# Performance work log

Measured on AMD Instinct MI355X. Metric: run time of the kernel, lower is better.

The kernel has to match this reference:

```python
import jax, jax.numpy as jnp
import numpy as np

N_QUBITS = 20
BATCH = 16


def setup_inputs() -> dict:
    key = jax.random.key(0)
    k1, k2 = jax.random.split(key)
    phi = jax.random.normal(k1, (BATCH, 2 ** N_QUBITS), dtype=jnp.float32)
    thetas = jax.random.normal(k2, (BATCH, N_QUBITS), dtype=jnp.float32)
    return {"phi": phi, "thetas": thetas}


def reference(phi, thetas):
    """Apply per-qubit RX(theta) rotations to the state vector.

    phi: [B, 2**n] real float32 initial amplitudes (cast to complex64).
    thetas: [B, n] rotation angles, qubit 0 = most-significant bit
    (matches torch view([B] + [2]*n) axis ordering, applied sequentially).
    Returns real/imag stacked: [B, 2**n, 2] float32.
    """
    B, S = phi.shape
    n = N_QUBITS
    c = jnp.cos(thetas / 2).astype(jnp.complex64)          # [B, n]
    s = (-1j * jnp.sin(thetas / 2)).astype(jnp.complex64)  # [B, n]
    state = phi.astype(jnp.complex64)                      # [B, S]
    for i in range(n):  # fixed small loop over qubits (butterfly stages)
        left = 2 ** i
        right = S // (2 * left)
        st = state.reshape(B, left, 2, right)
        a = st[:, :, 0, :]
        b = st[:, :, 1, :]
        ci = c[:, i, None, None]
        si = s[:, i, None, None]
        na = ci * a + si * b
        nb = si * a + ci * b
        state = jnp.stack([na, nb], axis=2).reshape(B, S)
    return jnp.stack([state.real, state.imag], axis=-1)
```

## Files before the change

kernel.cpp:

```cpp
#include <hip/hip_runtime.h>
#include <hip/hip_fp16.h>

#define NQ 20

__device__ __forceinline__ float bcast_first(float x) {
    return __int_as_float(__builtin_amdgcn_readfirstlane(__float_as_int(x)));
}

__device__ __forceinline__ void bfly(float C, float SV, float2& a, float2& b) {
    float2 na = make_float2(C * a.x + SV * b.y, C * a.y - SV * b.x);
    float2 nb = make_float2(C * b.x + SV * a.y, C * b.y - SV * a.x);
    a = na; b = nb;
}

__device__ __forceinline__ void bfly4(float C, float SV, float4& a, float4& b) {
    float4 na = make_float4(C*a.x + SV*b.y, C*a.y - SV*b.x, C*a.z + SV*b.w, C*a.w - SV*b.z);
    float4 nb = make_float4(C*b.x + SV*a.y, C*b.y - SV*a.x, C*b.z + SV*a.w, C*b.w - SV*a.z);
    a = na; b = nb;
}

__device__ __forceinline__ unsigned int pack_h2(float re, float im) {
    __half2 h = __floats2half2_rn(re, im);
    return *(unsigned int*)&h;
}
__device__ __forceinline__ float2 unpack_h2(unsigned int u) {
    return __half22float2(*(__half2*)&u);
}

__device__ __forceinline__ int swz1(int l) { return l ^ (((l >> 7) & 7) << 2); }

__global__ void rx_trig(const float* __restrict__ thetas, float2* __restrict__ tab) {
    int i = threadIdx.x;
    if (i < 16 * NQ) {
        float th = 0.5f * thetas[i];
        tab[i] = make_float2(cosf(th), sinf(th));
    }
}

__global__ __launch_bounds__(64) void rx_pass1_h(
        const float* __restrict__ phi, const float2* __restrict__ tab,
        unsigned int* __restrict__ ws) {
    __shared__ unsigned int lds[2048];
    const int lane = threadIdx.x;
    const int W = blockIdx.x;
    const int b = W >> 9;
    const int base = (W & 511) << 11;
    const float* ph = phi + ((size_t)b << NQ) + base;
    unsigned int* wp = ws + ((size_t)b << NQ) + base;

    float c[11], sv[11];
#pragma unroll
    for (int beta = 0; beta < 11; ++beta) {
        float2 t = tab[b * NQ + (NQ - 1 - beta)];
        c[beta]  = bcast_first(t.x);
        sv[beta] = bcast_first(t.y);
    }

    float2 v[32];
#pragma unroll
    for (int k4 = 0; k4 < 8; ++k4) {
        float4 t = *(const float4*)(ph + (k4 << 8) + (lane << 2));
        v[k4 * 4 + 0] = make_float2(t.x, 0.f);
        v[k4 * 4 + 1] = make_float2(t.y, 0.f);
        v[k4 * 4 + 2] = make_float2(t.z, 0.f);
        v[k4 * 4 + 3] = make_float2(t.w, 0.f);
    }

    const int regbit1[5]  = {0, 1, 8, 9, 10};
    const int regmask1[5] = {1, 2, 4, 8, 16};
#pragma unroll
    for (int t = 0; t < 5; ++t) {
        const float C = c[regbit1[t]], SV = sv[regbit1[t]];
        const int m = regmask1[t];
#pragma unroll
        for (int r = 0; r < 32; ++r)
            if (!(r & m)) bfly(C, SV, v[r], v[r | m]);
    }

#pragma unroll
    for (int k4 = 0; k4 < 8; ++k4) {
        int s0 = swz1((k4 << 8) + (lane << 2));
        uint4 pk;
        pk.x = pack_h2(v[k4*4+0].x, v[k4*4+0].y);
        pk.y = pack_h2(v[k4*4+1].x, v[k4*4+1].y);
        pk.z = pack_h2(v[k4*4+2].x, v[k4*4+2].y);
        pk.w = pack_h2(v[k4*4+3].x, v[k4*4+3].y);
        *(uint4*)&lds[s0] = pk;
    }
    __syncthreads();

    const int g = lane >> 2, lam = lane & 3;
#pragma unroll
    for (int r = 0; r < 32; ++r)
        v[r] = unpack_h2(lds[swz1((g << 7) | (r << 2) | lam)]);

#pragma unroll
    for (int t = 0; t < 5; ++t) {
        const float C = c[2 + t], SV = sv[2 + t];
        const int m = 1 << t;
#pragma unroll
        for (int r = 0; r < 32; ++r)
            if (!(r & m)) bfly(C, SV, v[r], v[r | m]);
    }

    {
        const float C = c[7], SV = sv[7];
#pragma unroll
        for (int r = 0; r < 32; ++r) {
            float px = __shfl_xor(v[r].x, 4, 64);
            float py = __shfl_xor(v[r].y, 4, 64);
            v[r] = make_float2(C * v[r].x + SV * py, C * v[r].y - SV * px);
        }
    }

#pragma unroll
    for (int r = 0; r < 32; ++r)
        lds[swz1((g << 7) | (r << 2) | lam)] = pack_h2(v[r].x, v[r].y);
    __syncthreads();

#pragma unroll
    for (int k = 0; k < 8; ++k) {
        int l0 = ((lane & 31) << 2) | ((k & 1) << 7)
               | ((lane >> 5) << 8) | ((k >> 1) << 9);
        uint4 pk = *(uint4*)&lds[swz1(l0)];
        *(uint4*)(wp + l0) = pk;
    }
}

__device__ __forceinline__ int p2idx(int h, int g) {
    return (h << 6) + (((g ^ (h & 15)) & 15) << 2);
}

__global__ __launch_bounds__(1024, 4) void rx_pass2_h(
        const float2* __restrict__ tab, const unsigned int* __restrict__ ws,
        float2* __restrict__ out) {
    __shared__ unsigned int buf[32768];
    const int tid = threadIdx.x;
    const int b = blockIdx.x >> 5;
    const int lb = blockIdx.x & 31;
    const unsigned int* pin = ws + ((size_t)b << NQ) + (lb << 6);
    float2* pout = out + ((size_t)b << NQ) + (lb << 6);

    float c[9], sv[9];
#pragma unroll
    for (int i = 0; i < 9; ++i) {
        float2 t = tab[b * NQ + (8 - i)];
        c[i]  = bcast_first(t.x);
        sv[i] = bcast_first(t.y);
    }

#pragma unroll
    for (int i = 0; i < 8; ++i) {
        int f = (i << 10) | tid;
        int h = f >> 4, q = f & 15;
        uint4 t = *(const uint4*)(pin + h * 2048 + (q << 2));
        *(uint4*)&buf[p2idx(h, q)] = t;
    }
    __syncthreads();

    {
        const int hl = tid & 31;
        const int j  = tid >> 5;
        const int gg = j >> 1, off = (j & 1) << 1;
        float4 w[16];
#pragma unroll
        for (int m = 0; m < 16; ++m) {
            int h = (m << 5) | hl;
            uint2 t = *(const uint2*)&buf[p2idx(h, gg) + off];
            float2 a = unpack_h2(t.x), bb = unpack_h2(t.y);
            w[m] = make_float4(a.x, a.y, bb.x, bb.y);
        }
#pragma unroll
        for (int t = 0; t < 4; ++t) {
            const float C = c[5 + t], SV = sv[5 + t];
            const int msk = 1 << t;
#pragma unroll
            for (int m = 0; m < 16; ++m)
                if (!(m & msk)) bfly4(C, SV, w[m], w[m | msk]);
        }
#pragma unroll
        for (int m = 0; m < 16; ++m) {
            int h = (m << 5) | hl;
            uint2 t;
            t.x = pack_h2(w[m].x, w[m].y);
            t.y = pack_h2(w[m].z, w[m].w);
            *(uint2*)&buf[p2idx(h, gg) + off] = t;
        }
    }
    __syncthreads();

    {
        const int hh = tid >> 6;
        const int ll = tid & 63;
        const int gg = ll >> 2, off = ll & 3;
        float2 v[32];
#pragma unroll
        for (int r = 0; r < 32; ++r) {
            int h = (hh << 5) | r;
            v[r] = unpack_h2(buf[p2idx(h, gg) + off]);
        }
#pragma unroll
        for (int t = 0; t < 5; ++t) {
            const float C = c[t], SV = sv[t];
            const int msk = 1 << t;
#pragma unroll
            for (int r = 0; r < 32; ++r)
                if (!(r & msk)) bfly(C, SV, v[r], v[r | msk]);
        }
#pragma unroll
        for (int r = 0; r < 32; ++r) {
            int h = (hh << 5) | r;
            pout[h * 2048 + ll] = v[r];
        }
    }
}

__global__ __launch_bounds__(64) void rx_pass1(
        const float* __restrict__ phi, const float* __restrict__ thetas,
        float2* __restrict__ out) {
    __shared__ float2 lds[2048];
    const int lane = threadIdx.x;
    const int W = blockIdx.x;
    const int b = W >> 9;
    const int base = (W & 511) << 11;
    const float* ph = phi + ((size_t)b << NQ) + base;
    float2* op = out + ((size_t)b << NQ) + base;

    float c[11], sv[11];
#pragma unroll
    for (int beta = 0; beta < 11; ++beta) {
        float th = 0.5f * thetas[b * NQ + (NQ - 1 - beta)];
        c[beta]  = bcast_first(cosf(th));
        sv[beta] = bcast_first(sinf(th));
    }

    float2 v[32];
#pragma unroll
    for (int k4 = 0; k4 < 8; ++k4) {
        float4 t = *(const float4*)(ph + (k4 << 8) + (lane << 2));
        v[k4 * 4 + 0] = make_float2(t.x, 0.f);
        v[k4 * 4 + 1] = make_float2(t.y, 0.f);
        v[k4 * 4 + 2] = make_float2(t.z, 0.f);
        v[k4 * 4 + 3] = make_float2(t.w, 0.f);
    }

    const int regbit1[5]  = {0, 1, 8, 9, 10};
    const int regmask1[5] = {1, 2, 4, 8, 16};
#pragma unroll
    for (int t = 0; t < 5; ++t) {
        const float C = c[regbit1[t]], SV = sv[regbit1[t]];
        const int m = regmask1[t];
#pragma unroll
        for (int r = 0; r < 32; ++r)
            if (!(r & m)) bfly(C, SV, v[r], v[r | m]);
    }

#pragma unroll
    for (int k4 = 0; k4 < 8; ++k4) {
        int low0 = (k4 << 8) + (lane << 2);
        int s0 = swz1(low0);
        *(float4*)&lds[s0]     = make_float4(v[k4*4+0].x, v[k4*4+0].y, v[k4*4+1].x, v[k4*4+1].y);
        *(float4*)&lds[s0 + 2] = make_float4(v[k4*4+2].x, v[k4*4+2].y, v[k4*4+3].x, v[k4*4+3].y);
    }
    __syncthreads();

    {
        const int g = lane >> 2, lam = lane & 3;
        float2 w2[32];
#pragma unroll
        for (int r = 0; r < 32; ++r) {
            int l = (g << 7) | (r << 2) | lam;
            w2[r] = lds[swz1(l)];
        }
#pragma unroll
        for (int t = 0; t < 5; ++t) {
            const float C = c[2 + t], SV = sv[2 + t];
            const int m = 1 << t;
#pragma unroll
            for (int r = 0; r < 32; ++r)
                if (!(r & m)) bfly(C, SV, w2[r], w2[r | m]);
        }
#pragma unroll
        for (int r = 0; r < 32; ++r) {
            int l = (g << 7) | (r << 2) | lam;
            lds[swz1(l)] = w2[r];
        }
    }
    __syncthreads();

    float4 u[16];
#pragma unroll
    for (int m = 0; m < 16; ++m) {
        int l0 = (lane << 1) | ((m & 1) << 7) | (((m >> 1) & 1) << 8)
               | (((m >> 2) & 1) << 9) | (((m >> 3) & 1) << 10);
        u[m] = *(float4*)&lds[swz1(l0)];
    }
    {
        const float C = c[7], SV = sv[7];
#pragma unroll
        for (int m = 0; m < 16; m += 2) {
            float4 A = u[m], B = u[m + 1];
            u[m]     = make_float4(C*A.x + SV*B.y, C*A.y - SV*B.x, C*A.z + SV*B.w, C*A.w - SV*B.z);
            u[m + 1] = make_float4(C*B.x + SV*A.y, C*B.y - SV*A.x, C*B.z + SV*A.w, C*B.w - SV*A.z);
        }
    }
#pragma unroll
    for (int m = 0; m < 16; ++m) {
        int l0 = (lane << 1) | ((m & 1) << 7) | (((m >> 1) & 1) << 8)
               | (((m >> 2) & 1) << 9) | (((m >> 3) & 1) << 10);
        *(float4*)(op + l0) = u[m];
    }
}

__device__ __forceinline__ int ppos(int h, int q) {
    return (h << 4) + (((q ^ (h & 7) ^ ((h >> 5) & 7)) & 7) << 1);
}

__global__ __launch_bounds__(256) void rx_pass2(
        const float* __restrict__ thetas, float2* __restrict__ out) {
    __shared__ float2 buf[8192];
    const int tid = threadIdx.x;
    const int b = blockIdx.x >> 7;
    const int lb = blockIdx.x & 127;
    float2* p = out + ((size_t)b << NQ) + (lb << 4);

    float c[9], sv[9];
#pragma unroll
    for (int i = 0; i < 9; ++i) {
        float th = 0.5f * thetas[b * NQ + (8 - i)];
        c[i]  = bcast_first(cosf(th));
        sv[i] = bcast_first(sinf(th));
    }

#pragma unroll
    for (int i = 0; i < 16; ++i) {
        int f = (i << 8) | tid;
        int h = f >> 3, j = f & 7;
        float4 t = *(const float4*)(p + h * 2048 + (j << 1));
        *(float4*)&buf[ppos(h, j)] = t;
    }
    __syncthreads();

    {
        const int hl = tid & 31;
        const int j  = tid >> 5;
        float4 w[16];
#pragma unroll
        for (int m = 0; m < 16; ++m)
            w[m] = *(float4*)&buf[ppos((m << 5) | hl, j)];
#pragma unroll
        for (int t = 0; t < 4; ++t) {
            const float C = c[5 + t], SV = sv[5 + t];
            const int msk = 1 << t;
#pragma unroll
            for (int m = 0; m < 16; ++m)
                if (!(m & msk)) bfly4(C, SV, w[m], w[m | msk]);
        }
#pragma unroll
        for (int m = 0; m < 16; ++m)
            *(float4*)&buf[ppos((m << 5) | hl, j)] = w[m];
    }
    __syncthreads();

    {
        const int hh = tid >> 4;
        const int ll = tid & 15;
        float2 v[32];
#pragma unroll
        for (int r = 0; r < 32; ++r) {
            int h = (hh << 5) | r;
            v[r] = buf[ppos(h, ll >> 1) + (ll & 1)];
        }
#pragma unroll
        for (int t = 0; t < 5; ++t) {
            const float C = c[t], SV = sv[t];
            const int msk = 1 << t;
#pragma unroll
            for (int r = 0; r < 32; ++r)
                if (!(r & msk)) bfly(C, SV, v[r], v[r | msk]);
        }
#pragma unroll
        for (int r = 0; r < 32; ++r) {
            int h = (hh << 5) | r;
            p[h * 2048 + ll] = v[r];
        }
    }
}

extern "C" void kernel_launch(void* const* d_in, const int* in_sizes, int n_in,
                              void* d_out, int out_size, void* d_ws, size_t ws_size,
                              hipStream_t stream) {
    const float* phi    = (const float*)d_in[0];
    const float* thetas = (const float*)d_in[1];
    float2* out = (float2*)d_out;
    const size_t half_bytes = ((size_t)16 << NQ) * 4;
    const size_t need = half_bytes + 4096;
    if (d_ws != nullptr && ws_size >= need) {
        unsigned int* ws = (unsigned int*)d_ws;
        float2* tab = (float2*)((char*)d_ws + half_bytes);
        rx_trig<<<1, 320, 0, stream>>>(thetas, tab);
        rx_pass1_h<<<8192, 64, 0, stream>>>(phi, tab, ws);
        rx_pass2_h<<<512, 1024, 0, stream>>>(tab, ws, out);
    } else {
        rx_pass1<<<8192, 64, 0, stream>>>(phi, thetas, out);
        rx_pass2<<<2048, 256, 0, stream>>>(thetas, out);
    }
}
```

Before: 278.6 us.

## Reorder passes: apply high-qubit stages first into transposed fp16 intermediate

Swaps the order of the two fp16 passes. The first pass now reads phi as real values, applies the 9 high-order qubit rotations over 512-stride columns, and writes a per-block transposed tile layout. The second pass gathers contiguous tiles, applies the 11 low-order rotations, and writes the complex output with contiguous float4 stores. The intent is to make the final fp32 output write fully contiguous and to use larger blocks with fewer, bigger launches. The gather in the second pass now reads scattered 16-byte chunks from the intermediate, which may hurt coalescing.

```diff
diff --git a/kernel.cpp b/kernel.cpp
--- a/kernel.cpp
+++ b/kernel.cpp
@@ -37,16 +37,93 @@
     }
 }
 
-__global__ __launch_bounds__(64) void rx_pass1_h(
+__global__ __launch_bounds__(512, 4) void rx_hi(
         const float* __restrict__ phi, const float2* __restrict__ tab,
-        unsigned int* __restrict__ ws) {
-    __shared__ unsigned int lds[2048];
-    const int lane = threadIdx.x;
-    const int W = blockIdx.x;
-    const int b = W >> 9;
-    const int base = (W & 511) << 11;
-    const float* ph = phi + ((size_t)b << NQ) + base;
-    unsigned int* wp = ws + ((size_t)b << NQ) + base;
+        unsigned int* __restrict__ inter) {
+    __shared__ unsigned int T[512 * 32];
+    const int tid = threadIdx.x;
+    const int b  = blockIdx.x >> 6;
+    const int lb = blockIdx.x & 63;
+    const float* ph = phi + ((size_t)b << NQ) + (lb << 5);
+    unsigned int* tp = inter + ((size_t)blockIdx.x << 14);
+
+    float c[9], sv[9];
+#pragma unroll
+    for (int i = 0; i < 9; ++i) {
+        float2 t = tab[b * NQ + (8 - i)];
+        c[i]  = bcast_first(t.x);
+        sv[i] = bcast_first(t.y);
+    }
+
+#pragma unroll
+    for (int i = 0; i < 8; ++i) {
+        int f = (i << 9) | tid;
+        int h = f >> 3, q = f & 7;
+        float4 t = *(const float4*)(ph + h * 2048 + (q << 2));
+        uint4 pk;
+        pk.x = pack_h2(t.x, 0.f);
+        pk.y = pack_h2(t.y, 0.f);
+        pk.z = pack_h2(t.z, 0.f);
+        pk.w = pack_h2(t.w, 0.f);
+        *(uint4*)&T[(h << 5) + (q << 2)] = pk;
+    }
+    __syncthreads();
+
+    {
+        const int hg = tid >> 5, ll = tid & 31;
+        float2 v[32];
+#pragma unroll
+        for (int r = 0; r < 32; ++r)
+            v[r] = unpack_h2(T[((hg << 5) + r) * 32 + ll]);
+#pragma unroll
+        for (int t = 0; t < 5; ++t) {
+            const float C = c[t], SV = sv[t];
+            const int m = 1 << t;
+#pragma unroll
+            for (int r = 0; r < 32; ++r)
+                if (!(r & m)) bfly(C, SV, v[r], v[r | m]);
+        }
+#pragma unroll
+        for (int r = 0; r < 32; ++r)
+            T[((hg << 5) + r) * 32 + ll] = pack_h2(v[r].x, v[r].y);
+    }
+    __syncthreads();
+
+    {
+        const int u = tid >> 4, llp = tid & 15;
+        float4 w[16];
+#pragma unroll
+        for (int r2 = 0; r2 < 16; ++r2) {
+            uint2 t2 = *(uint2*)&T[((u + (r2 << 5)) << 5) + (llp << 1)];
+            float2 a = unpack_h2(t2.x), bb = unpack_h2(t2.y);
+            w[r2] = make_float4(a.x, a.y, bb.x, bb.y);
+        }
+#pragma unroll
+        for (int t = 0; t < 4; ++t) {
+            const float C = c[5 + t], SV = sv[5 + t];
+            const int m = 1 << t;
+#pragma unroll
+            for (int r2 = 0; r2 < 16; ++r2)
+                if (!(r2 & m)) bfly4(C, SV, w[r2], w[r2 | m]);
+        }
+#pragma unroll
+        for (int r2 = 0; r2 < 16; ++r2) {
+            uint2 pk;
+            pk.x = pack_h2(w[r2].x, w[r2].y);
+            pk.y = pack_h2(w[r2].z, w[r2].w);
+            *(uint2*)(tp + ((u + (r2 << 5)) << 5) + (llp << 1)) = pk;
+        }
+    }
+}
+
+__global__ __launch_bounds__(512, 4) void rx_lo(
+        const float2* __restrict__ tab, const unsigned int* __restrict__ inter,
+        float2* __restrict__ out) {
+    __shared__ unsigned int T[8 * 2048];
+    const int tid = threadIdx.x;
+    const int b   = blockIdx.x >> 6;
+    const int h0  = (blockIdx.x & 63) << 3;
+    float2* op = out + ((size_t)b << NQ) + ((size_t)h0 << 11);
 
     float c[11], sv[11];
 #pragma unroll
@@ -56,14 +133,28 @@
         sv[beta] = bcast_first(t.y);
     }
 
+#pragma unroll
+    for (int i = 0; i < 8; ++i) {
+        int f = (i << 9) | tid;
+        int hh = f >> 9, rp = f & 511;
+        int lb = rp >> 3, q = rp & 7;
+        uint4 t = *(const uint4*)(inter + (((size_t)(b << 6) + lb) << 14)
+                                  + ((h0 + hh) << 5) + (q << 2));
+        *(uint4*)&T[(hh << 11) + swz1(rp << 2)] = t;
+    }
+    __syncthreads();
+
+    const int hh = tid >> 6, lane = tid & 63;
+    unsigned int* R = &T[hh << 11];
+
     float2 v[32];
 #pragma unroll
     for (int k4 = 0; k4 < 8; ++k4) {
-        float4 t = *(const float4*)(ph + (k4 << 8) + (lane << 2));
-        v[k4 * 4 + 0] = make_float2(t.x, 0.f);
-        v[k4 * 4 + 1] = make_float2(t.y, 0.f);
-        v[k4 * 4 + 2] = make_float2(t.z, 0.f);
-        v[k4 * 4 + 3] = make_float2(t.w, 0.f);
+        uint4 tq = *(uint4*)&R[swz1((k4 << 8) + (lane << 2))];
+        v[k4 * 4 + 0] = unpack_h2(tq.x);
+        v[k4 * 4 + 1] = unpack_h2(tq.y);
+        v[k4 * 4 + 2] = unpack_h2(tq.z);
+        v[k4 * 4 + 3] = unpack_h2(tq.w);
     }
 
     const int regbit1[5]  = {0, 1, 8, 9, 10};
@@ -79,20 +170,18 @@
 
 #pragma unroll
     for (int k4 = 0; k4 < 8; ++k4) {
-        int s0 = swz1((k4 << 8) + (lane << 2));
         uint4 pk;
         pk.x = pack_h2(v[k4*4+0].x, v[k4*4+0].y);
         pk.y = pack_h2(v[k4*4+1].x, v[k4*4+1].y);
         pk.z = pack_h2(v[k4*4+2].x, v[k4*4+2].y);
         pk.w = pack_h2(v[k4*4+3].x, v[k4*4+3].y);
-        *(uint4*)&lds[s0] = pk;
-    }
-    __syncthreads();
+        *(uint4*)&R[swz1((k4 << 8) + (lane << 2))] = pk;
+    }
 
     const int g = lane >> 2, lam = lane & 3;
 #pragma unroll
     for (int r = 0; r < 32; ++r)
-        v[r] = unpack_h2(lds[swz1((g << 7) | (r << 2) | lam)]);
+        v[r] = unpack_h2(R[swz1((g << 7) | (r << 2) | lam)]);
 
 #pragma unroll
     for (int t = 0; t < 5; ++t) {
@@ -115,103 +204,14 @@
 
 #pragma unroll
     for (int r = 0; r < 32; ++r)
-        lds[swz1((g << 7) | (r << 2) | lam)] = pack_h2(v[r].x, v[r].y);
-    __syncthreads();
-
-#pragma unroll
-    for (int k = 0; k < 8; ++k) {
-        int l0 = ((lane & 31) << 2) | ((k & 1) << 7)
-               | ((lane >> 5) << 8) | ((k >> 1) << 9);
-        uint4 pk = *(uint4*)&lds[swz1(l0)];
-        *(uint4*)(wp + l0) = pk;
-    }
-}
-
-__device__ __forceinline__ int p2idx(int h, int g) {
-    return (h << 6) + (((g ^ (h & 15)) & 15) << 2);
-}
-
-__global__ __launch_bounds__(1024, 4) void rx_pass2_h(
-        const float2* __restrict__ tab, const unsigned int* __restrict__ ws,
-        float2* __restrict__ out) {
-    __shared__ unsigned int buf[32768];
-    const int tid = threadIdx.x;
-    const int b = blockIdx.x >> 5;
-    const int lb = blockIdx.x & 31;
-    const unsigned int* pin = ws + ((size_t)b << NQ) + (lb << 6);
-    float2* pout = out + ((size_t)b << NQ) + (lb << 6);
-
-    float c[9], sv[9];
-#pragma unroll
-    for (int i = 0; i < 9; ++i) {
-        float2 t = tab[b * NQ + (8 - i)];
-        c[i]  = bcast_first(t.x);
-        sv[i] = bcast_first(t.y);
-    }
-
-#pragma unroll
-    for (int i = 0; i < 8; ++i) {
-        int f = (i << 10) | tid;
-        int h = f >> 4, q = f & 15;
-        uint4 t = *(const uint4*)(pin + h * 2048 + (q << 2));
-        *(uint4*)&buf[p2idx(h, q)] = t;
-    }
-    __syncthreads();
-
-    {
-        const int hl = tid & 31;
-        const int j  = tid >> 5;
-        const int gg = j >> 1, off = (j & 1) << 1;
-        float4 w[16];
-#pragma unroll
-        for (int m = 0; m < 16; ++m) {
-            int h = (m << 5) | hl;
-            uint2 t = *(const uint2*)&buf[p2idx(h, gg) + off];
-            float2 a = unpack_h2(t.x), bb = unpack_h2(t.y);
-            w[m] = make_float4(a.x, a.y, bb.x, bb.y);
-        }
-#pragma unroll
-        for (int t = 0; t < 4; ++t) {
-            const float C = c[5 + t], SV = sv[5 + t];
-            const int msk = 1 << t;
-#pragma unroll
-            for (int m = 0; m < 16; ++m)
-                if (!(m & msk)) bfly4(C, SV, w[m], w[m | msk]);
-        }
-#pragma unroll
-        for (int m = 0; m < 16; ++m) {
-            int h = (m << 5) | hl;
-            uint2 t;
-            t.x = pack_h2(w[m].x, w[m].y);
-            t.y = pack_h2(w[m].z, w[m].w);
-            *(uint2*)&buf[p2idx(h, gg) + off] = t;
-        }
-    }
-    __syncthreads();
-
-    {
-        const int hh = tid >> 6;
-        const int ll = tid & 63;
-        const int gg = ll >> 2, off = ll & 3;
-        float2 v[32];
-#pragma unroll
-        for (int r = 0; r < 32; ++r) {
-            int h = (hh << 5) | r;
-            v[r] = unpack_h2(buf[p2idx(h, gg) + off]);
-        }
-#pragma unroll
-        for (int t = 0; t < 5; ++t) {
-            const float C = c[t], SV = sv[t];
-            const int msk = 1 << t;
-#pragma unroll
-            for (int r = 0; r < 32; ++r)
-                if (!(r & msk)) bfly(C, SV, v[r], v[r | msk]);
-        }
-#pragma unroll
-        for (int r = 0; r < 32; ++r) {
-            int h = (hh << 5) | r;
-            pout[h * 2048 + ll] = v[r];
-        }
+        R[swz1((g << 7) | (r << 2) | lam)] = pack_h2(v[r].x, v[r].y);
+
+#pragma unroll
+    for (int k = 0; k < 16; ++k) {
+        int j0 = (k << 7) | (lane << 1);
+        uint2 t2 = *(uint2*)&R[swz1(j0)];
+        float2 a = unpack_h2(t2.x), bb = unpack_h2(t2.y);
+        *(float4*)(op + ((size_t)hh << 11) + j0) = make_float4(a.x, a.y, bb.x, bb.y);
     }
 }
 
@@ -224,7 +224,7 @@
     const int b = W >> 9;
     const int base = (W & 511) << 11;
     const float* ph = phi + ((size_t)b << NQ) + base;
-    float2* op = out + ((size_t)b << NQ) + base;
+    float2* opp = out + ((size_t)b << NQ) + base;
 
     float c[11], sv[11];
 #pragma unroll
@@ -257,8 +257,7 @@
 
 #pragma unroll
     for (int k4 = 0; k4 < 8; ++k4) {
-        int low0 = (k4 << 8) + (lane << 2);
-        int s0 = swz1(low0);
+        int s0 = swz1((k4 << 8) + (lane << 2));
         *(float4*)&lds[s0]     = make_float4(v[k4*4+0].x, v[k4*4+0].y, v[k4*4+1].x, v[k4*4+1].y);
         *(float4*)&lds[s0 + 2] = make_float4(v[k4*4+2].x, v[k4*4+2].y, v[k4*4+3].x, v[k4*4+3].y);
     }
@@ -268,10 +267,8 @@
         const int g = lane >> 2, lam = lane & 3;
         float2 w2[32];
 #pragma unroll
-        for (int r = 0; r < 32; ++r) {
-            int l = (g << 7) | (r << 2) | lam;
-            w2[r] = lds[swz1(l)];
-        }
+        for (int r = 0; r < 32; ++r)
+            w2[r] = lds[swz1((g << 7) | (r << 2) | lam)];
 #pragma unroll
         for (int t = 0; t < 5; ++t) {
             const float C = c[2 + t], SV = sv[2 + t];
@@ -281,10 +278,8 @@
                 if (!(r & m)) bfly(C, SV, w2[r], w2[r | m]);
         }
 #pragma unroll
-        for (int r = 0; r < 32; ++r) {
-            int l = (g << 7) | (r << 2) | lam;
-            lds[swz1(l)] = w2[r];
-        }
+        for (int r = 0; r < 32; ++r)
+            lds[swz1((g << 7) | (r << 2) | lam)] = w2[r];
     }
     __syncthreads();
 
@@ -308,7 +303,7 @@
     for (int m = 0; m < 16; ++m) {
         int l0 = (lane << 1) | ((m & 1) << 7) | (((m >> 1) & 1) << 8)
                | (((m >> 2) & 1) << 9) | (((m >> 3) & 1) << 10);
-        *(float4*)(op + l0) = u[m];
+        *(float4*)(opp + l0) = u[m];
     }
 }
 
@@ -367,10 +362,8 @@
         const int ll = tid & 15;
         float2 v[32];
 #pragma unroll
-        for (int r = 0; r < 32; ++r) {
-            int h = (hh << 5) | r;
-            v[r] = buf[ppos(h, ll >> 1) + (ll & 1)];
-        }
+        for (int r = 0; r < 32; ++r)
+            v[r] = buf[ppos((hh << 5) | r, ll >> 1) + (ll & 1)];
 #pragma unroll
         for (int t = 0; t < 5; ++t) {
             const float C = c[t], SV = sv[t];
@@ -380,10 +373,8 @@
                 if (!(r & msk)) bfly(C, SV, v[r], v[r | msk]);
         }
 #pragma unroll
-        for (int r = 0; r < 32; ++r) {
-            int h = (hh << 5) | r;
-            p[h * 2048 + ll] = v[r];
-        }
+        for (int r = 0; r < 32; ++r)
+            p[((hh << 5) | r) * 2048 + ll] = v[r];
     }
 }
 
@@ -396,11 +387,11 @@
     const size_t half_bytes = ((size_t)16 << NQ) * 4;
     const size_t need = half_bytes + 4096;
     if (d_ws != nullptr && ws_size >= need) {
-        unsigned int* ws = (unsigned int*)d_ws;
+        unsigned int* inter = (unsigned int*)d_ws;
         float2* tab = (float2*)((char*)d_ws + half_bytes);
         rx_trig<<<1, 320, 0, stream>>>(thetas, tab);
-        rx_pass1_h<<<8192, 64, 0, stream>>>(phi, tab, ws);
-        rx_pass2_h<<<512, 1024, 0, stream>>>(tab, ws, out);
+        rx_hi<<<1024, 512, 0, stream>>>(phi, tab, inter);
+        rx_lo<<<1024, 512, 0, stream>>>(tab, inter, out);
     } else {
         rx_pass1<<<8192, 64, 0, stream>>>(phi, thetas, out);
         rx_pass2<<<2048, 256, 0, stream>>>(thetas, out);
```

Result: slower. 367.3 us (+31.8%).
